# Kernel optimization log

Hardware: AMD Instinct MI355X
Metric: run time of the kernel (lower is better)

## Reference

```python
import jax, jax.numpy as jnp
from jax import lax
import numpy as np

NPOINT = 1024
RADIUS = 0.1
NSAMPLE = 32
BN_EPS = 1e-5


def _fps(xyz, npoint):
    # xyz: [B, N, 3]. Deterministic start at index 0 (torch uses randint seed).
    B, N, _ = xyz.shape

    def step(carry, _):
        dist, far = carry
        centroid = jnp.take_along_axis(xyz, far[:, None, None], axis=1)  # [B,1,3]
        d = jnp.sum((xyz - centroid) ** 2, axis=-1)                      # [B,N]
        dist = jnp.minimum(dist, d)
        nxt = jnp.argmax(dist, axis=-1).astype(jnp.int32)
        return (dist, nxt), far

    init = (jnp.full((B, N), 1e10, xyz.dtype), jnp.zeros((B,), jnp.int32))
    _, idx = lax.scan(step, init, None, length=npoint)
    return jnp.transpose(idx)  # [B, npoint]


def _sqdist(a, b):
    # a: [B,S,3], b: [B,N,3] -> [B,S,N]
    return (jnp.sum(a * a, -1)[:, :, None] + jnp.sum(b * b, -1)[:, None, :]
            - 2.0 * jnp.einsum('bsc,bnc->bsn', a, b))


def _gather(pts, idx):
    # pts: [B,N,C], idx: [B,...] int -> [B,...,C]
    B = pts.shape[0]
    flat = idx.reshape(B, -1)
    out = jnp.take_along_axis(pts, flat[..., None], axis=1)
    return out.reshape(idx.shape + (pts.shape[-1],))


def _ball_query(radius, nsample, xyz, new_xyz):
    B, N, _ = xyz.shape
    sq = _sqdist(new_xyz, xyz)                                        # [B,S,N]
    ar = jnp.arange(N, dtype=jnp.int32)[None, None, :]
    gi = jnp.where(sq > radius ** 2, N, ar)                           # out-of-ball -> N
    gi = jnp.sort(gi, axis=-1)[:, :, :nsample]                        # [B,S,K]
    first = gi[:, :, :1]
    return jnp.where(gi == N, first, gi)                              # pad with first


def _sa_forward(xyz, points, params):
    # torch layout in: xyz [B,3,N], points [B,D,N]
    xyz = jnp.transpose(xyz, (0, 2, 1))        # [B,N,3]
    points = jnp.transpose(points, (0, 2, 1))  # [B,N,D]
    fps_idx = lax.stop_gradient(_fps(xyz, NPOINT))          # [B,S]
    new_xyz = _gather(xyz, fps_idx)                          # [B,S,3]
    idx = _ball_query(RADIUS, NSAMPLE, xyz, new_xyz)         # [B,S,K]
    g_xyz = _gather(xyz, idx) - new_xyz[:, :, None, :]       # [B,S,K,3]
    g_pts = _gather(points, idx)                             # [B,S,K,D]
    x = jnp.concatenate([g_xyz, g_pts], axis=-1)             # [B,S,K,3+D]
    for (W, b, g, bt, m, v) in params:
        x = jnp.einsum('bskc,oc->bsko', x, W) + b            # 1x1 conv
        x = (x - m) * (g / jnp.sqrt(v + BN_EPS)) + bt        # eval-mode BN
        x = jax.nn.relu(x)
    feat = jnp.max(x, axis=2)                                # max over K -> [B,S,C']
    return jnp.transpose(feat, (0, 2, 1))                    # [B,C',S]


def setup_inputs() -> dict:
    key = jax.random.key(0)
    ks = jax.random.split(key, 16)
    B, N = 4, 8192
    d = {}
    d['xyz'] = jax.random.uniform(ks[0], (B, 3, N), jnp.float32)       # unit cube cloud
    d['points'] = jax.random.normal(ks[1], (B, 3, N), jnp.float32)     # e.g. normals
    dims = [(6, 64), (64, 64), (64, 128)]
    k = 2
    for li, (cin, cout) in enumerate(dims, start=1):
        d[f'w{li}'] = jax.random.normal(ks[k], (cout, cin), jnp.float32) * (1.0 / np.sqrt(cin)); k += 1
        d[f'b{li}'] = jnp.zeros((cout,), jnp.float32)
        d[f'g{li}'] = jnp.ones((cout,), jnp.float32)
        d[f't{li}'] = jnp.zeros((cout,), jnp.float32)
        d[f'm{li}'] = jax.random.normal(ks[k], (cout,), jnp.float32) * 0.01; k += 1
        d[f'v{li}'] = jnp.ones((cout,), jnp.float32)
    return d


def reference(xyz, points,
              w1, b1, g1, t1, m1, v1,
              w2, b2, g2, t2, m2, v2,
              w3, b3, g3, t3, m3, v3):
    params = [(w1, b1, g1, t1, m1, v1),
              (w2, b2, g2, t2, m2, v2),
              (w3, b3, g3, t3, m3, v3)]
    return _sa_forward(xyz, points, params)
```

## Files before the change

### kernel.cpp

```cpp
#include <hip/hip_runtime.h>
#include <math.h>

#define NPTS 8192
#define NPOINT 1024
#define NSAMPLE 32

typedef float v2f __attribute__((ext_vector_type(2)));

template <int CTRL>
__device__ __forceinline__ float dpp_fmax_step(float v) {
  int s = __builtin_amdgcn_update_dpp(0, __float_as_int(v), CTRL, 0xF, 0xF, true);
  return fmaxf(v, __int_as_float(s));
}
template <int CTRL>
__device__ __forceinline__ unsigned dpp_umax_step(unsigned v) {
  int s = __builtin_amdgcn_update_dpp(0, (int)v, CTRL, 0xF, 0xF, true);
  unsigned u = (unsigned)s;
  return (u > v) ? u : v;
}

__global__ __launch_bounds__(256, 1) void fps_kernel(const float4* __restrict__ xyz4,
                                                     float* __restrict__ new_xyz) {
#pragma clang fp contract(off)
  const int b = blockIdx.x;
  const int tid = threadIdx.x;
  const float4* xp4 = xyz4 + (size_t)b * NPTS;
  v2f px2[16], py2[16], pz2[16], d2[16];
#pragma unroll
  for (int j = 0; j < 16; ++j) {
    int n0 = tid + 512 * j;
    float4 a = xp4[n0];
    float4 c2 = xp4[n0 + 256];
    px2[j] = (v2f){a.x, c2.x};
    py2[j] = (v2f){a.y, c2.y};
    pz2[j] = (v2f){a.z, c2.z};
    d2[j] = (v2f){1e10f, 1e10f};
  }
  __shared__ unsigned long long red[2][4];
  float* outp = new_xyz + (size_t)b * NPOINT * 3;
  float4 c0 = xp4[0];
  float cx = c0.x, cy = c0.y, cz = c0.z;
  if (tid == 0) { outp[0] = cx; outp[1] = cy; outp[2] = cz; }
  for (int s = 1; s < NPOINT; ++s) {
    const v2f cxx = (v2f){cx, cx};
    const v2f cyy = (v2f){cy, cy};
    const v2f czz = (v2f){cz, cz};
    float bv = -1.0f;
    int bI = 0;
#pragma unroll
    for (int j = 0; j < 16; ++j) {
      v2f dx = px2[j] - cxx;
      v2f dy = py2[j] - cyy;
      v2f dz = pz2[j] - czz;
      v2f xx = dx * dx;
      v2f yy = dy * dy;
      v2f zz = dz * dz;
      v2f d = (xx + yy) + zz;
      float dmx = fminf(d2[j].x, d.x);
      float dmy = fminf(d2[j].y, d.y);
      d2[j].x = dmx;
      d2[j].y = dmy;
      if (dmx > bv) { bv = dmx; bI = 2 * j; }
      if (dmy > bv) { bv = dmy; bI = 2 * j + 1; }
    }
    int bi = tid + (bI << 8);
    float m = bv;
    m = dpp_fmax_step<0x111>(m);
    m = dpp_fmax_step<0x112>(m);
    m = dpp_fmax_step<0x114>(m);
    m = dpp_fmax_step<0x118>(m);
    m = dpp_fmax_step<0x142>(m);
    m = dpp_fmax_step<0x143>(m);
    float Mw = __int_as_float(__builtin_amdgcn_readlane(__float_as_int(m), 63));
    unsigned k2 = (bv == Mw) ? (unsigned)(8191 - bi) : 0u;
    k2 = dpp_umax_step<0x111>(k2);
    k2 = dpp_umax_step<0x112>(k2);
    k2 = dpp_umax_step<0x114>(k2);
    k2 = dpp_umax_step<0x118>(k2);
    k2 = dpp_umax_step<0x142>(k2);
    k2 = dpp_umax_step<0x143>(k2);
    unsigned K2 = (unsigned)__builtin_amdgcn_readlane((int)k2, 63);
    unsigned long long wkey =
        ((unsigned long long)__float_as_uint(Mw) << 32) | K2;
    if ((tid & 63) == 0) red[s & 1][tid >> 6] = wkey;
    __syncthreads();
    unsigned long long k0 = red[s & 1][0];
    unsigned long long k1 = red[s & 1][1];
    unsigned long long kB = red[s & 1][2];
    unsigned long long k3 = red[s & 1][3];
    unsigned long long ka = (k0 > k1) ? k0 : k1;
    unsigned long long kb = (kB > k3) ? kB : k3;
    unsigned long long km = (ka > kb) ? ka : kb;
    int gi = 8191 - (int)(unsigned)(km & 0xFFFFFFFFull);
    int giu = __builtin_amdgcn_readfirstlane(gi);
    float4 cc = xp4[giu];
    cx = cc.x; cy = cc.y; cz = cc.z;
    if (tid == 0) { outp[3 * s] = cx; outp[3 * s + 1] = cy; outp[3 * s + 2] = cz; }
  }
}

__global__ __launch_bounds__(256) void bq_kernel(const float* __restrict__ xyz,
                                                 const float* __restrict__ new_xyz,
                                                 int* __restrict__ idx_out) {
#pragma clang fp contract(off)
  __shared__ int slots[4][NSAMPLE];
  const int tid = threadIdx.x;
  const int wv = tid >> 6, lane = tid & 63;
  const int gc = blockIdx.x * 4 + wv;
  const int b = gc >> 10;
  const float* xp = xyz + (size_t)b * 3 * NPTS;
  const float* cp = new_xyz + (size_t)gc * 3;
  const float cx = cp[0], cy = cp[1], cz = cp[2];
  const float asq = (cx * cx + cy * cy) + cz * cz;
  int cnt = 0;
  for (int base = 0; base < NPTS; base += 64) {
    int n = base + lane;
    float x = xp[n], y = xp[NPTS + n], z = xp[2 * NPTS + n];
    float bsq = (x * x + y * y) + z * z;
    float ab = (x * cx + y * cy) + z * cz;
    float sq = (asq + bsq) - 2.0f * ab;
    bool inc = !(sq > 0.01f);
    unsigned long long mk = __ballot(inc);
    int pos = cnt + (int)__popcll(mk & ((1ull << lane) - 1ull));
    if (inc && pos < NSAMPLE) slots[wv][pos] = n;
    cnt += (int)__popcll(mk);
    if (cnt >= NSAMPLE) break;
  }
  __syncthreads();
  if (lane < NSAMPLE) {
    int first = slots[wv][0];
    int v = (lane < cnt) ? slots[wv][lane] : first;
    idx_out[(size_t)gc * NSAMPLE + lane] = v;
  }
}

__global__ __launch_bounds__(256) void setup_kernel(
    const float* __restrict__ xyz, const float* __restrict__ w3,
    const float* __restrict__ b1, const float* __restrict__ g1, const float* __restrict__ t1,
    const float* __restrict__ m1, const float* __restrict__ v1,
    const float* __restrict__ b2, const float* __restrict__ g2, const float* __restrict__ t2,
    const float* __restrict__ m2, const float* __restrict__ v2,
    const float* __restrict__ b3, const float* __restrict__ g3, const float* __restrict__ t3,
    const float* __restrict__ m3, const float* __restrict__ v3,
    float4* __restrict__ xyz4, float* __restrict__ w3t, float* __restrict__ scsh) {
  int tid = threadIdx.x;
  int p = blockIdx.x * 256 + tid;
  int bb = p >> 13, n = p & 8191;
  const float* src = xyz + (size_t)bb * 3 * NPTS;
  xyz4[p] = make_float4(src[n], src[NPTS + n], src[2 * NPTS + n], 0.f);
  if (blockIdx.x != 0) return;
  for (int i = tid; i < 8192; i += 256) {
    int o = i >> 6, c = i & 63;
    w3t[c * 128 + o] = w3[i];
  }
  if (tid < 64) {
    float s = g1[tid] / sqrtf(v1[tid] + 1e-5f);
    scsh[tid] = s;
    scsh[64 + tid] = (b1[tid] - m1[tid]) * s + t1[tid];
    float s2 = g2[tid] / sqrtf(v2[tid] + 1e-5f);
    scsh[128 + tid] = s2;
    scsh[192 + tid] = (b2[tid] - m2[tid]) * s2 + t2[tid];
  }
  if (tid < 128) {
    float s3 = g3[tid] / sqrtf(v3[tid] + 1e-5f);
    scsh[256 + tid] = s3;
    scsh[384 + tid] = (b3[tid] - m3[tid]) * s3 + t3[tid];
  }
}

__global__ __launch_bounds__(256, 2) void mlp_kernel(
    const float* __restrict__ xyz, const float* __restrict__ points,
    const float* __restrict__ new_xyz, const int* __restrict__ idx,
    const float* __restrict__ w1, const float* __restrict__ w2,
    const float* __restrict__ w3t, const float* __restrict__ scsh,
    float* __restrict__ out) {
  __shared__ float act[256 * 64];
  float4* act4 = (float4*)act;
  const int tid = threadIdx.x;
  const int s0 = blockIdx.x * 8;
  const int b = s0 >> 10;
  const int g = tid >> 5;
  const int k = tid & 31;
  const int gc = s0 + g;
  const float* xp = xyz + (size_t)b * 3 * NPTS;
  const float* pp = points + (size_t)b * 3 * NPTS;
  const float* cp = new_xyz + (size_t)gc * 3;
  const int n = idx[(size_t)gc * NSAMPLE + k];
  float f0 = xp[n] - cp[0];
  float f1 = xp[NPTS + n] - cp[1];
  float f2 = xp[2 * NPTS + n] - cp[2];
  float f3 = pp[n];
  float f4 = pp[NPTS + n];
  float f5 = pp[2 * NPTS + n];
  const float* sc1 = scsh;        const float* sh1 = scsh + 64;
  const float* sc2 = scsh + 128;  const float* sh2 = scsh + 192;
  const float* sc3 = scsh + 256;  const float* sh3 = scsh + 384;
  const int row = tid;

#pragma unroll
  for (int oc = 0; oc < 16; ++oc) {
    float va[4];
#pragma unroll
    for (int jj = 0; jj < 4; ++jj) {
      int o = oc * 4 + jj;
      const float* wr = w1 + o * 6;
      float a = f0 * wr[0] + f1 * wr[1] + f2 * wr[2] +
                f3 * wr[3] + f4 * wr[4] + f5 * wr[5];
      va[jj] = fmaxf(a * sc1[o] + sh1[o], 0.f);
    }
    act4[row * 16 + (oc ^ (row & 15))] = make_float4(va[0], va[1], va[2], va[3]);
  }

  float acc[64];
#pragma unroll
  for (int o = 0; o < 64; ++o) acc[o] = 0.f;
  for (int cc = 0; cc < 16; ++cc) {
    float4 av = act4[row * 16 + (cc ^ (row & 15))];
#pragma unroll
    for (int o = 0; o < 64; ++o) {
      const float* wr = w2 + o * 64 + cc * 4;
      acc[o] += av.x * wr[0] + av.y * wr[1] + av.z * wr[2] + av.w * wr[3];
    }
  }
#pragma unroll
  for (int oc = 0; oc < 16; ++oc) {
    float va[4];
#pragma unroll
    for (int jj = 0; jj < 4; ++jj) {
      int o = oc * 4 + jj;
      va[jj] = fmaxf(acc[o] * sc2[o] + sh2[o], 0.f);
    }
    act4[row * 16 + (oc ^ (row & 15))] = make_float4(va[0], va[1], va[2], va[3]);
  }
  __syncthreads();

  const int j = k;
  const int sb = gc & 1023;
  for (int p = 0; p < 4; ++p) {
    int o3 = p * 32 + j;
    float wreg[64];
#pragma unroll
    for (int c = 0; c < 64; ++c) wreg[c] = w3t[c * 128 + o3];
    float osc = sc3[o3], osh = sh3[o3];
    float vmax = 0.f;
    for (int kk = 0; kk < 32; ++kk) {
      int r2 = g * 32 + kk;
      float a0 = 0.f, a1 = 0.f, a2 = 0.f, a3 = 0.f;
#pragma unroll
      for (int cc = 0; cc < 16; cc += 4) {
        float4 u0 = act4[r2 * 16 + ((cc + 0) ^ (r2 & 15))];
        float4 u1 = act4[r2 * 16 + ((cc + 1) ^ (r2 & 15))];
        float4 u2 = act4[r2 * 16 + ((cc + 2) ^ (r2 & 15))];
        float4 u3 = act4[r2 * 16 + ((cc + 3) ^ (r2 & 15))];
        a0 += u0.x * wreg[4*cc+0]  + u0.y * wreg[4*cc+1]  + u0.z * wreg[4*cc+2]  + u0.w * wreg[4*cc+3];
        a1 += u1.x * wreg[4*cc+4]  + u1.y * wreg[4*cc+5]  + u1.z * wreg[4*cc+6]  + u1.w * wreg[4*cc+7];
        a2 += u2.x * wreg[4*cc+8]  + u2.y * wreg[4*cc+9]  + u2.z * wreg[4*cc+10] + u2.w * wreg[4*cc+11];
        a3 += u3.x * wreg[4*cc+12] + u3.y * wreg[4*cc+13] + u3.z * wreg[4*cc+14] + u3.w * wreg[4*cc+15];
      }
      float x3 = (a0 + a1) + (a2 + a3);
      vmax = fmaxf(vmax, fmaxf(x3 * osc + osh, 0.f));
    }
    out[((size_t)b * 128 + o3) * 1024 + sb] = vmax;
  }
}

extern "C" void kernel_launch(void* const* d_in, const int* in_sizes, int n_in,
                              void* d_out, int out_size, void* d_ws, size_t ws_size,
                              hipStream_t stream) {
  (void)in_sizes; (void)n_in; (void)out_size; (void)ws_size;
  const float* xyz    = (const float*)d_in[0];
  const float* points = (const float*)d_in[1];
  const float* w1 = (const float*)d_in[2];
  const float* b1 = (const float*)d_in[3];
  const float* g1 = (const float*)d_in[4];
  const float* t1 = (const float*)d_in[5];
  const float* m1 = (const float*)d_in[6];
  const float* v1 = (const float*)d_in[7];
  const float* w2 = (const float*)d_in[8];
  const float* b2 = (const float*)d_in[9];
  const float* g2 = (const float*)d_in[10];
  const float* t2 = (const float*)d_in[11];
  const float* m2 = (const float*)d_in[12];
  const float* v2 = (const float*)d_in[13];
  const float* w3 = (const float*)d_in[14];
  const float* b3 = (const float*)d_in[15];
  const float* g3 = (const float*)d_in[16];
  const float* t3 = (const float*)d_in[17];
  const float* m3 = (const float*)d_in[18];
  const float* v3 = (const float*)d_in[19];

  float* wsf = (float*)d_ws;
  float* new_xyz = wsf;
  int*   idx     = (int*)(wsf + 12288);
  float* w3t     = wsf + 12288 + 131072;
  float* scsh    = w3t + 8192;
  float4* xyz4   = (float4*)(scsh + 512);
  float* out     = (float*)d_out;

  hipLaunchKernelGGL(setup_kernel, dim3(128), dim3(256), 0, stream,
                     xyz, w3, b1, g1, t1, m1, v1, b2, g2, t2, m2, v2,
                     b3, g3, t3, m3, v3, xyz4, w3t, scsh);
  hipLaunchKernelGGL(fps_kernel, dim3(4), dim3(256), 0, stream, xyz4, new_xyz);
  hipLaunchKernelGGL(bq_kernel, dim3(1024), dim3(256), 0, stream,
                     xyz, new_xyz, idx);
  hipLaunchKernelGGL(mlp_kernel, dim3(512), dim3(256), 0, stream,
                     xyz, points, new_xyz, idx, w1, w2, w3t, scsh, out);
}
```

Before: 1.247 ms.

## Fuse ball query into MLP kernel and streamline FPS argmax reduction

```diff
diff --git a/kernel.cpp b/kernel.cpp
--- a/kernel.cpp
+++ b/kernel.cpp
@@ -11,12 +11,6 @@
 __device__ __forceinline__ float dpp_fmax_step(float v) {
   int s = __builtin_amdgcn_update_dpp(0, __float_as_int(v), CTRL, 0xF, 0xF, true);
   return fmaxf(v, __int_as_float(s));
-}
-template <int CTRL>
-__device__ __forceinline__ unsigned dpp_umax_step(unsigned v) {
-  int s = __builtin_amdgcn_update_dpp(0, (int)v, CTRL, 0xF, 0xF, true);
-  unsigned u = (unsigned)s;
-  return (u > v) ? u : v;
 }
 
 __global__ __launch_bounds__(256, 1) void fps_kernel(const float4* __restrict__ xyz4,
@@ -37,10 +31,10 @@
     d2[j] = (v2f){1e10f, 1e10f};
   }
   __shared__ unsigned long long red[2][4];
-  float* outp = new_xyz + (size_t)b * NPOINT * 3;
+  __shared__ float4 ctab[NPOINT];
   float4 c0 = xp4[0];
   float cx = c0.x, cy = c0.y, cz = c0.z;
-  if (tid == 0) { outp[0] = cx; outp[1] = cy; outp[2] = cz; }
+  if (tid == 0) ctab[0] = c0;
   for (int s = 1; s < NPOINT; ++s) {
     const v2f cxx = (v2f){cx, cx};
     const v2f cyy = (v2f){cy, cy};
@@ -72,17 +66,24 @@
     m = dpp_fmax_step<0x142>(m);
     m = dpp_fmax_step<0x143>(m);
     float Mw = __int_as_float(__builtin_amdgcn_readlane(__float_as_int(m), 63));
-    unsigned k2 = (bv == Mw) ? (unsigned)(8191 - bi) : 0u;
-    k2 = dpp_umax_step<0x111>(k2);
-    k2 = dpp_umax_step<0x112>(k2);
-    k2 = dpp_umax_step<0x114>(k2);
-    k2 = dpp_umax_step<0x118>(k2);
-    k2 = dpp_umax_step<0x142>(k2);
-    k2 = dpp_umax_step<0x143>(k2);
-    unsigned K2 = (unsigned)__builtin_amdgcn_readlane((int)k2, 63);
-    unsigned long long wkey =
-        ((unsigned long long)__float_as_uint(Mw) << 32) | K2;
-    if ((tid & 63) == 0) red[s & 1][tid >> 6] = wkey;
+    unsigned long long mask = __ballot(bv == Mw);
+    int bi_w;
+    if (__popcll(mask) == 1) {
+      bi_w = __builtin_amdgcn_readlane(bi, (int)(__ffsll(mask) - 1));
+    } else {
+      bi_w = NPTS;
+      unsigned long long mm = mask;
+      while (mm) {
+        int l = (int)(__ffsll(mm) - 1);
+        int bb = __builtin_amdgcn_readlane(bi, l);
+        bi_w = (bb < bi_w) ? bb : bi_w;
+        mm &= (mm - 1);
+      }
+    }
+    unsigned long long key =
+        ((unsigned long long)__float_as_uint(Mw) << 32) |
+        (unsigned)(8191 - bi_w);
+    if ((tid & 63) == 0) red[s & 1][tid >> 6] = key;
     __syncthreads();
     unsigned long long k0 = red[s & 1][0];
     unsigned long long k1 = red[s & 1][1];
@@ -95,42 +96,13 @@
     int giu = __builtin_amdgcn_readfirstlane(gi);
     float4 cc = xp4[giu];
     cx = cc.x; cy = cc.y; cz = cc.z;
-    if (tid == 0) { outp[3 * s] = cx; outp[3 * s + 1] = cy; outp[3 * s + 2] = cz; }
-  }
-}
-
-__global__ __launch_bounds__(256) void bq_kernel(const float* __restrict__ xyz,
-                                                 const float* __restrict__ new_xyz,
-                                                 int* __restrict__ idx_out) {
-#pragma clang fp contract(off)
-  __shared__ int slots[4][NSAMPLE];
-  const int tid = threadIdx.x;
-  const int wv = tid >> 6, lane = tid & 63;
-  const int gc = blockIdx.x * 4 + wv;
-  const int b = gc >> 10;
-  const float* xp = xyz + (size_t)b * 3 * NPTS;
-  const float* cp = new_xyz + (size_t)gc * 3;
-  const float cx = cp[0], cy = cp[1], cz = cp[2];
-  const float asq = (cx * cx + cy * cy) + cz * cz;
-  int cnt = 0;
-  for (int base = 0; base < NPTS; base += 64) {
-    int n = base + lane;
-    float x = xp[n], y = xp[NPTS + n], z = xp[2 * NPTS + n];
-    float bsq = (x * x + y * y) + z * z;
-    float ab = (x * cx + y * cy) + z * cz;
-    float sq = (asq + bsq) - 2.0f * ab;
-    bool inc = !(sq > 0.01f);
-    unsigned long long mk = __ballot(inc);
-    int pos = cnt + (int)__popcll(mk & ((1ull << lane) - 1ull));
-    if (inc && pos < NSAMPLE) slots[wv][pos] = n;
-    cnt += (int)__popcll(mk);
-    if (cnt >= NSAMPLE) break;
+    if (tid == 0) ctab[s] = cc;
   }
   __syncthreads();
-  if (lane < NSAMPLE) {
-    int first = slots[wv][0];
-    int v = (lane < cnt) ? slots[wv][lane] : first;
-    idx_out[(size_t)gc * NSAMPLE + lane] = v;
+  float* outp = new_xyz + (size_t)b * NPOINT * 3;
+  for (int i = tid; i < NPOINT; i += 256) {
+    float4 c = ctab[i];
+    outp[3 * i] = c.x; outp[3 * i + 1] = c.y; outp[3 * i + 2] = c.z;
   }
 }
 
@@ -170,13 +142,14 @@
 
 __global__ __launch_bounds__(256, 2) void mlp_kernel(
     const float* __restrict__ xyz, const float* __restrict__ points,
-    const float* __restrict__ new_xyz, const int* __restrict__ idx,
+    const float* __restrict__ new_xyz,
     const float* __restrict__ w1, const float* __restrict__ w2,
     const float* __restrict__ w3t, const float* __restrict__ scsh,
     float* __restrict__ out) {
   __shared__ float act[256 * 64];
   float4* act4 = (float4*)act;
   const int tid = threadIdx.x;
+  const int wv = tid >> 6, lane = tid & 63;
   const int s0 = blockIdx.x * 8;
   const int b = s0 >> 10;
   const int g = tid >> 5;
@@ -184,8 +157,39 @@
   const int gc = s0 + g;
   const float* xp = xyz + (size_t)b * 3 * NPTS;
   const float* pp = points + (size_t)b * 3 * NPTS;
+
+  int* slots = (int*)(act + wv * 4096);
+  {
+#pragma clang fp contract(off)
+    for (int h = 0; h < 2; ++h) {
+      const int hc = s0 + 2 * wv + h;
+      const float* cp0 = new_xyz + (size_t)hc * 3;
+      const float cx = cp0[0], cy = cp0[1], cz = cp0[2];
+      const float asq = (cx * cx + cy * cy) + cz * cz;
+      int cnt = 0;
+      for (int base = 0; base < NPTS; base += 64) {
+        int n = base + lane;
+        float x = xp[n], y = xp[NPTS + n], z = xp[2 * NPTS + n];
+        float bsq = (x * x + y * y) + z * z;
+        float ab = (x * cx + y * cy) + z * cz;
+        float sq = (asq + bsq) - 2.0f * ab;
+        bool inc = !(sq > 0.01f);
+        unsigned long long mk = __ballot(inc);
+        int pos = cnt + (int)__popcll(mk & ((1ull << lane) - 1ull));
+        if (inc && pos < NSAMPLE) slots[h * 32 + pos] = n;
+        cnt += (int)__popcll(mk);
+        if (cnt >= NSAMPLE) break;
+      }
+      if (lane < NSAMPLE) {
+        int first = slots[h * 32];
+        int v = (lane < cnt) ? slots[h * 32 + lane] : first;
+        slots[h * 32 + lane] = v;
+      }
+    }
+  }
+  const int n = slots[(g & 1) * 32 + k];
+
   const float* cp = new_xyz + (size_t)gc * 3;
-  const int n = idx[(size_t)gc * NSAMPLE + k];
   float f0 = xp[n] - cp[0];
   float f1 = xp[NPTS + n] - cp[1];
   float f2 = xp[2 * NPTS + n] - cp[2];
@@ -291,8 +295,7 @@
 
   float* wsf = (float*)d_ws;
   float* new_xyz = wsf;
-  int*   idx     = (int*)(wsf + 12288);
-  float* w3t     = wsf + 12288 + 131072;
+  float* w3t     = wsf + 12288;
   float* scsh    = w3t + 8192;
   float4* xyz4   = (float4*)(scsh + 512);
   float* out     = (float*)d_out;
@@ -301,8 +304,6 @@
                      xyz, w3, b1, g1, t1, m1, v1, b2, g2, t2, m2, v2,
                      b3, g3, t3, m3, v3, xyz4, w3t, scsh);
   hipLaunchKernelGGL(fps_kernel, dim3(4), dim3(256), 0, stream, xyz4, new_xyz);
-  hipLaunchKernelGGL(bq_kernel, dim3(1024), dim3(256), 0, stream,
-                     xyz, new_xyz, idx);
   hipLaunchKernelGGL(mlp_kernel, dim3(512), dim3(256), 0, stream,
-                     xyz, points, new_xyz, idx, w1, w2, w3t, scsh, out);
-}
+                     xyz, points, new_xyz, w1, w2, w3t, scsh, out);
+}
```

Result: no change. 1.263 ms (+1.3%).
